# Kernel optimization log

Measured on AMD Instinct MI355X. Metric: run time of the kernel, lower is better.

Reference implementation:

```python
import jax, jax.numpy as jnp
import numpy as np

B, T, D = 16, 512, 256
HS, D_A, R = 512, 64, 8


def setup_inputs() -> dict:
    key = jax.random.key(0)
    ks = jax.random.split(key, 8)
    s = lambda *sh: 1.0 / np.sqrt(sh[0])
    x = jax.random.normal(ks[0], (B, T, D), dtype=jnp.float32)
    w_first = jax.random.normal(ks[1], (D, D_A), dtype=jnp.float32) * s(D)
    b_first = jnp.zeros((D_A,), dtype=jnp.float32)
    w_second = jax.random.normal(ks[2], (D_A, R), dtype=jnp.float32) * s(D_A)
    b_second = jnp.zeros((R,), dtype=jnp.float32)
    weight_iBarh = jax.random.normal(ks[3], (D, 4 * HS), dtype=jnp.float32) * s(D)
    weight_hh = jax.random.normal(ks[4], (HS, 4 * HS), dtype=jnp.float32) * s(HS)
    bias = jnp.zeros((4 * HS,), dtype=jnp.float32)
    return {"x": x, "w_first": w_first, "b_first": b_first,
            "w_second": w_second, "b_second": b_second,
            "weight_iBarh": weight_iBarh, "weight_hh": weight_hh, "bias": bias}


def _forward(x, w_first, b_first, w_second, b_second, weight_iBarh, weight_hh, bias):
    b, t, d = x.shape
    hs = weight_hh.shape[0]
    r = w_second.shape[1]
    # attention logits for every timestep: (B, T, r)
    s = jnp.tanh(x @ w_first + b_first) @ w_second + b_second
    # causal mask: query t attends to keys j <= t
    mask = jnp.tril(jnp.ones((t, t), dtype=bool))  # (t_query, j_key)
    # logits: (B, Tq, Tk, r); softmax over key axis per (t, r), masked to prefix
    logits = jnp.where(mask[None, :, :, None], s[:, None, :, :], -jnp.inf)
    attn = jax.nn.softmax(logits, axis=2).mean(axis=-1)  # (B, Tq, Tk) == mean over r
    # M_t = attention-weighted average of prefix inputs: (B, T, D)
    M = jnp.einsum('btj,bjd->btd', attn, x)
    gates_x = jnp.einsum('btd,dg->btg', M, weight_iBarh) + bias  # (B, T, 4H)

    def step(carry, gx):
        h, c = carry
        g = gx + h @ weight_hh  # (B, 4H)
        i = jax.nn.sigmoid(g[:, :hs])
        f = jax.nn.sigmoid(g[:, hs:2 * hs])
        gg = jnp.tanh(g[:, 2 * hs:3 * hs])
        o = jax.nn.sigmoid(g[:, 3 * hs:])
        c = f * c + i * gg
        h = o * jnp.tanh(c)
        return (h, c), h

    h0 = jnp.zeros((b, hs), dtype=x.dtype)
    c0 = jnp.zeros((b, hs), dtype=x.dtype)
    (h_t, c_t), hseq = jax.lax.scan(step, (h0, c0), jnp.swapaxes(gates_x, 0, 1))
    hidden_seq = jnp.swapaxes(hseq, 0, 1)  # (B, T, H)
    return hidden_seq, h_t, c_t


def reference(x, w_first, b_first, w_second, b_second, weight_iBarh, weight_hh, bias):
    return _forward(x, w_first, b_first, w_second, b_second, weight_iBarh, weight_hh, bias)
```

## Files before the change

### kernel.cpp

```cpp
#include <hip/hip_runtime.h>
#include <math.h>

#define BB 16
#define TT 512
#define DD 256
#define HS 512
#define DA 64
#define RR 8
#define G4H 2048


__global__ __launch_bounds__(256) void k1_score(
    const float* __restrict__ x, const float* __restrict__ w1,
    const float* __restrict__ b1, const float* __restrict__ w2,
    const float* __restrict__ b2, float* __restrict__ s_out) {
  const int wave = threadIdx.x >> 6;
  const int lane = threadIdx.x & 63;
  for (int i = 0; i < 4; ++i) {
    const int bt = blockIdx.x * 16 + wave * 4 + i;
    const float* xr = x + bt * DD;
    float acc = b1[lane];
    #pragma unroll 4
    for (int d = 0; d < DD; ++d)
      acc = fmaf(xr[d], w1[d * DA + lane], acc);
    const float a = tanhf(acc);
    #pragma unroll
    for (int r = 0; r < RR; ++r) {
      float v = a * w2[lane * RR + r];
      for (int off = 32; off > 0; off >>= 1) v += __shfl_xor(v, off);
      if (lane == 0) s_out[bt * RR + r] = v + b2[r];
    }
  }
}

__global__ __launch_bounds__(512) void k2_prefix(
    const float* __restrict__ s_in, float* __restrict__ e_out,
    float* __restrict__ inv_out) {
  const int b = blockIdx.x >> 3, r = blockIdx.x & 7;
  const int t = threadIdx.x;
  __shared__ float red[TT];
  __shared__ float buf[2][TT];
  const float v = s_in[(b * TT + t) * RR + r];
  red[t] = v;
  __syncthreads();
  for (int off = 256; off >= 1; off >>= 1) {
    if (t < off) red[t] = fmaxf(red[t], red[t + off]);
    __syncthreads();
  }
  const float m = red[0];
  const float e = expf(v - m);
  int p = 0;
  buf[0][t] = e;
  __syncthreads();
  for (int off = 1; off < TT; off <<= 1) {
    const float add = (t >= off) ? buf[p][t - off] : 0.f;
    buf[1 - p][t] = buf[p][t] + add;
    __syncthreads();
    p ^= 1;
  }
  const float den = buf[p][t];
  e_out[(b * TT + t) * RR + r] = e;
  inv_out[(b * TT + t) * RR + r] = 1.0f / den;
}

__global__ __launch_bounds__(64) void k3_mix(
    const float* __restrict__ x, const float* __restrict__ e_in,
    const float* __restrict__ inv_in, float* __restrict__ Mout) {
  const int b = blockIdx.x >> 2;
  const int d = (blockIdx.x & 3) * 64 + threadIdx.x;
  __shared__ __align__(16) float el[TT * RR];
  __shared__ __align__(16) float il[TT * RR];
  for (int i = threadIdx.x * 4; i < TT * RR; i += 64 * 4) {
    *(float4*)&el[i] = *(const float4*)&e_in[b * TT * RR + i];
    *(float4*)&il[i] = *(const float4*)&inv_in[b * TT * RR + i];
  }
  __syncthreads();
  float4 c0 = {0.f, 0.f, 0.f, 0.f}, c1 = {0.f, 0.f, 0.f, 0.f};
  for (int t = 0; t < TT; ++t) {
    const float xv = x[(b * TT + t) * DD + d];
    const float4 e0 = *(const float4*)&el[t * RR];
    const float4 e1 = *(const float4*)&el[t * RR + 4];
    const float4 i0 = *(const float4*)&il[t * RR];
    const float4 i1 = *(const float4*)&il[t * RR + 4];
    c0.x = fmaf(e0.x, xv, c0.x); c0.y = fmaf(e0.y, xv, c0.y);
    c0.z = fmaf(e0.z, xv, c0.z); c0.w = fmaf(e0.w, xv, c0.w);
    c1.x = fmaf(e1.x, xv, c1.x); c1.y = fmaf(e1.y, xv, c1.y);
    c1.z = fmaf(e1.z, xv, c1.z); c1.w = fmaf(e1.w, xv, c1.w);
    float msum = c0.x * i0.x + c0.y * i0.y + c0.z * i0.z + c0.w * i0.w;
    msum += c1.x * i1.x + c1.y * i1.y + c1.z * i1.z + c1.w * i1.w;
    Mout[(b * TT + t) * DD + d] = msum * 0.125f;
  }
}

__global__ __launch_bounds__(256) void k4_gemm(
    const float* __restrict__ A, const float* __restrict__ Bw,
    const float* __restrict__ bias, float* __restrict__ C) {
  const int bn = blockIdx.x & 15;
  const int bm = blockIdx.x >> 4;
  const int tid = threadIdx.x;
  const int tx = tid & 15, ty = tid >> 4;
  __shared__ __align__(16) float As[16][132];
  __shared__ __align__(16) float Bs[16][132];
  const int row0 = bm * 128, col0 = bn * 128;

  float acc[2][4][2][4];
  #pragma unroll
  for (int a = 0; a < 2; ++a)
    #pragma unroll
    for (int i = 0; i < 4; ++i)
      #pragma unroll
      for (int q = 0; q < 2; ++q)
        #pragma unroll
        for (int j = 0; j < 4; ++j) acc[a][i][q][j] = 0.f;

  const int arow = tid >> 1, akc = (tid & 1) * 8;
  const int bkr = tid >> 4, bcc = (tid & 15) * 8;

  for (int k0 = 0; k0 < 256; k0 += 16) {
    const float4 a0 = *(const float4*)&A[(row0 + arow) * 256 + k0 + akc];
    const float4 a1 = *(const float4*)&A[(row0 + arow) * 256 + k0 + akc + 4];
    const float4 b0 = *(const float4*)&Bw[(k0 + bkr) * 2048 + col0 + bcc];
    const float4 b1 = *(const float4*)&Bw[(k0 + bkr) * 2048 + col0 + bcc + 4];
    __syncthreads();
    As[akc + 0][arow] = a0.x; As[akc + 1][arow] = a0.y;
    As[akc + 2][arow] = a0.z; As[akc + 3][arow] = a0.w;
    As[akc + 4][arow] = a1.x; As[akc + 5][arow] = a1.y;
    As[akc + 6][arow] = a1.z; As[akc + 7][arow] = a1.w;
    *(float4*)&Bs[bkr][bcc] = b0;
    *(float4*)&Bs[bkr][bcc + 4] = b1;
    __syncthreads();
    #pragma unroll
    for (int kk = 0; kk < 16; ++kk) {
      float av[8], bv[8];
      *(float4*)&av[0] = *(const float4*)&As[kk][ty * 4];
      *(float4*)&av[4] = *(const float4*)&As[kk][64 + ty * 4];
      *(float4*)&bv[0] = *(const float4*)&Bs[kk][tx * 4];
      *(float4*)&bv[4] = *(const float4*)&Bs[kk][64 + tx * 4];
      #pragma unroll
      for (int a = 0; a < 2; ++a)
        #pragma unroll
        for (int i = 0; i < 4; ++i)
          #pragma unroll
          for (int q = 0; q < 2; ++q)
            #pragma unroll
            for (int j = 0; j < 4; ++j)
              acc[a][i][q][j] = fmaf(av[a * 4 + i], bv[q * 4 + j], acc[a][i][q][j]);
    }
  }
  const float4 bias0 = *(const float4*)&bias[col0 + tx * 4];
  const float4 bias1 = *(const float4*)&bias[col0 + 64 + tx * 4];
  #pragma unroll
  for (int a = 0; a < 2; ++a)
    #pragma unroll
    for (int i = 0; i < 4; ++i) {
      const int row = row0 + a * 64 + ty * 4 + i;
      float4 v0, v1;
      v0.x = acc[a][i][0][0] + bias0.x; v0.y = acc[a][i][0][1] + bias0.y;
      v0.z = acc[a][i][0][2] + bias0.z; v0.w = acc[a][i][0][3] + bias0.w;
      v1.x = acc[a][i][1][0] + bias1.x; v1.y = acc[a][i][1][1] + bias1.y;
      v1.z = acc[a][i][1][2] + bias1.z; v1.w = acc[a][i][1][3] + bias1.w;
      *(float4*)&C[row * 2048 + col0 + tx * 4] = v0;
      *(float4*)&C[row * 2048 + col0 + 64 + tx * 4] = v1;
    }
}

#define FMA4(ACC, W4, HSC)                         \
  ACC.x = fmaf((W4).x, (HSC), ACC.x);              \
  ACC.y = fmaf((W4).y, (HSC), ACC.y);              \
  ACC.z = fmaf((W4).z, (HSC), ACC.z);              \
  ACC.w = fmaf((W4).w, (HSC), ACC.w);

__device__ __forceinline__ float fast_sigmoid(float x) {
  return __builtin_amdgcn_rcpf(1.f + __expf(-x));
}
__device__ __forceinline__ float fast_tanh(float x) {
  const float xc = fmaxf(x, -30.f);
  const float e = __expf(-2.f * xc);
  return (1.f - e) * __builtin_amdgcn_rcpf(1.f + e);
}

__global__ __launch_bounds__(512, 1) void k5_lstm(
    const float* __restrict__ gates, const float* __restrict__ whh,
    float* __restrict__ out, unsigned long long* hbuf) {
  const int s   = blockIdx.x & 15;
  const int b   = blockIdx.x >> 4;
  const int tid = threadIdx.x;
  const int kq  = tid & 15;
  const int cq  = tid >> 4;
  const int j0  = s * 32;
  const int unit = j0 + cq;

  __shared__ __align__(16) float Wl[256 * 128];
  __shared__ __align__(16) float hl[2][576];

  float4 wr[32];
  for (int rnd = 0; rnd < 2; ++rnd) {
    for (int i = tid * 4; i < 256 * 128; i += 512 * 4) {
      const int k = i >> 7, c = i & 127;
      *(float4*)&Wl[i] =
          *(const float4*)&whh[(rnd * 256 + k) * G4H + (c >> 5) * HS + j0 + (c & 31)];
    }
    __syncthreads();
    if ((kq >> 3) == rnd) {
      const int kb = (kq & 7) * 32;
      #pragma unroll
      for (int kk = 0; kk < 32; ++kk) {
        const int base = (kb + kk) * 128 + cq;
        wr[kk].x = *(volatile const float*)&Wl[base];
        wr[kk].y = *(volatile const float*)&Wl[base + 32];
        wr[kk].z = *(volatile const float*)&Wl[base + 64];
        wr[kk].w = *(volatile const float*)&Wl[base + 96];
      }
    }
    __syncthreads();
  }

  float c_reg = 0.f;

  for (int t = 0; t < TT; ++t) {
    float gi = 0.f, gf = 0.f, gg = 0.f, go = 0.f;
    if (kq == 0) {
      const float* gt = gates + ((long)b * TT + t) * G4H + unit;
      gi = gt[0]; gf = gt[HS]; gg = gt[2 * HS]; go = gt[3 * HS];
    }
    const int par = t & 1;
    if (t > 0) {
      const unsigned long long* hsrc = hbuf + (((t - 1) & 1) * BB + b) * HS;
      unsigned long long pkt;
      do {
        pkt = __hip_atomic_load(&hsrc[tid], __ATOMIC_RELAXED,
                                __HIP_MEMORY_SCOPE_AGENT);
      } while ((unsigned)(pkt >> 32) < (unsigned)t);
      hl[par][(tid >> 5) * 36 + (tid & 31)] = __uint_as_float((unsigned)pkt);
    }
    __syncthreads();
    float4 acc = {0.f, 0.f, 0.f, 0.f};
    if (t > 0) {
      const float* hb = &hl[par][kq * 36];
      #pragma unroll
      for (int i = 0; i < 8; ++i) {
        const float4 h4 = *(const float4*)(hb + i * 4);
        FMA4(acc, wr[i * 4 + 0], h4.x);
        FMA4(acc, wr[i * 4 + 1], h4.y);
        FMA4(acc, wr[i * 4 + 2], h4.z);
        FMA4(acc, wr[i * 4 + 3], h4.w);
      }
    }
    #pragma unroll
    for (int off = 1; off <= 8; off <<= 1) {
      acc.x += __shfl_xor(acc.x, off); acc.y += __shfl_xor(acc.y, off);
      acc.z += __shfl_xor(acc.z, off); acc.w += __shfl_xor(acc.w, off);
    }
    if (kq == 0) {
      const float I = fast_sigmoid(acc.x + gi);
      const float F = fast_sigmoid(acc.y + gf);
      const float G = fast_tanh(acc.z + gg);
      const float O = fast_sigmoid(acc.w + go);
      c_reg = F * c_reg + I * G;
      const float h = O * fast_tanh(c_reg);
      const unsigned long long pkt =
          ((unsigned long long)(unsigned)(t + 1) << 32) |
          (unsigned long long)__float_as_uint(h);
      __hip_atomic_store(&hbuf[((t & 1) * BB + b) * HS + unit], pkt,
                         __ATOMIC_RELAXED, __HIP_MEMORY_SCOPE_AGENT);
      out[((long)b * TT + t) * HS + unit] = h;
      if (t == TT - 1) {
        out[(long)BB * TT * HS + b * HS + unit] = h;
        out[(long)BB * TT * HS + BB * HS + b * HS + unit] = c_reg;
      }
    }
  }
}

extern "C" void kernel_launch(void* const* d_in, const int* in_sizes, int n_in,
                              void* d_out, int out_size, void* d_ws,
                              size_t ws_size, hipStream_t stream) {
  const float* x    = (const float*)d_in[0];
  const float* w1   = (const float*)d_in[1];
  const float* b1   = (const float*)d_in[2];
  const float* w2   = (const float*)d_in[3];
  const float* b2   = (const float*)d_in[4];
  const float* wih  = (const float*)d_in[5];
  const float* whh  = (const float*)d_in[6];
  const float* bias = (const float*)d_in[7];
  float* out = (float*)d_out;

  float* ws = (float*)d_ws;
  float* s_buf  = ws;
  float* e_buf  = ws + 65536;
  float* i_buf  = ws + 131072;
  float* M_buf  = ws + 196608;
  float* g_buf  = ws + 2293760;
  unsigned long long* hbuf64 = (unsigned long long*)ws;

  k1_score<<<512, 256, 0, stream>>>(x, w1, b1, w2, b2, s_buf);
  k2_prefix<<<BB * RR, 512, 0, stream>>>(s_buf, e_buf, i_buf);
  k3_mix<<<64, 64, 0, stream>>>(x, e_buf, i_buf, M_buf);
  k4_gemm<<<64 * 16, 256, 0, stream>>>(M_buf, wih, bias, g_buf);
  hipMemsetAsync(hbuf64, 0, 2 * BB * HS * sizeof(unsigned long long), stream);
  k5_lstm<<<256, 512, 0, stream>>>(g_buf, whh, out, hbuf64);
}
```

Measured before the change: 1.143 ms.

## Pipeline LSTM gate prefetch, overlap poll loads, use packed f2 FMAs

```diff
diff --git a/kernel.cpp b/kernel.cpp
--- a/kernel.cpp
+++ b/kernel.cpp
@@ -8,6 +8,8 @@
 #define DA 64
 #define RR 8
 #define G4H 2048
+
+typedef __attribute__((ext_vector_type(2))) float f2;
 
 
 __global__ __launch_bounds__(256) void k1_score(
@@ -164,12 +166,6 @@
     }
 }
 
-#define FMA4(ACC, W4, HSC)                         \
-  ACC.x = fmaf((W4).x, (HSC), ACC.x);              \
-  ACC.y = fmaf((W4).y, (HSC), ACC.y);              \
-  ACC.z = fmaf((W4).z, (HSC), ACC.z);              \
-  ACC.w = fmaf((W4).w, (HSC), ACC.w);
-
 __device__ __forceinline__ float fast_sigmoid(float x) {
   return __builtin_amdgcn_rcpf(1.f + __expf(-x));
 }
@@ -177,6 +173,11 @@
   const float xc = fmaxf(x, -30.f);
   const float e = __expf(-2.f * xc);
   return (1.f - e) * __builtin_amdgcn_rcpf(1.f + e);
+}
+
+__device__ __forceinline__ unsigned long long poll_ld(
+    const unsigned long long* p) {
+  return __hip_atomic_load(p, __ATOMIC_RELAXED, __HIP_MEMORY_SCOPE_AGENT);
 }
 
 __global__ __launch_bounds__(512, 1) void k5_lstm(
@@ -193,7 +194,7 @@
   __shared__ __align__(16) float Wl[256 * 128];
   __shared__ __align__(16) float hl[2][576];
 
-  float4 wr[32];
+  f2 wrA[32], wrB[32];
   for (int rnd = 0; rnd < 2; ++rnd) {
     for (int i = tid * 4; i < 256 * 128; i += 512 * 4) {
       const int k = i >> 7, c = i & 127;
@@ -206,10 +207,10 @@
       #pragma unroll
       for (int kk = 0; kk < 32; ++kk) {
         const int base = (kb + kk) * 128 + cq;
-        wr[kk].x = *(volatile const float*)&Wl[base];
-        wr[kk].y = *(volatile const float*)&Wl[base + 32];
-        wr[kk].z = *(volatile const float*)&Wl[base + 64];
-        wr[kk].w = *(volatile const float*)&Wl[base + 96];
+        wrA[kk].x = *(volatile const float*)&Wl[base];
+        wrA[kk].y = *(volatile const float*)&Wl[base + 32];
+        wrB[kk].x = *(volatile const float*)&Wl[base + 64];
+        wrB[kk].y = *(volatile const float*)&Wl[base + 96];
       }
     }
     __syncthreads();
@@ -217,51 +218,69 @@
 
   float c_reg = 0.f;
 
+  float4 g_cur = {0, 0, 0, 0}, g_n1 = {0, 0, 0, 0};
+  const float* gbase = gates + (long)b * TT * G4H + unit;
+  if (kq == 0) {
+    g_cur.x = gbase[0];            g_cur.y = gbase[HS];
+    g_cur.z = gbase[2 * HS];       g_cur.w = gbase[3 * HS];
+    const float* g1 = gbase + G4H;
+    g_n1.x = g1[0];                g_n1.y = g1[HS];
+    g_n1.z = g1[2 * HS];           g_n1.w = g1[3 * HS];
+  }
+
   for (int t = 0; t < TT; ++t) {
-    float gi = 0.f, gf = 0.f, gg = 0.f, go = 0.f;
-    if (kq == 0) {
-      const float* gt = gates + ((long)b * TT + t) * G4H + unit;
-      gi = gt[0]; gf = gt[HS]; gg = gt[2 * HS]; go = gt[3 * HS];
-    }
     const int par = t & 1;
     if (t > 0) {
-      const unsigned long long* hsrc = hbuf + (((t - 1) & 1) * BB + b) * HS;
-      unsigned long long pkt;
-      do {
-        pkt = __hip_atomic_load(&hsrc[tid], __ATOMIC_RELAXED,
-                                __HIP_MEMORY_SCOPE_AGENT);
-      } while ((unsigned)(pkt >> 32) < (unsigned)t);
-      hl[par][(tid >> 5) * 36 + (tid & 31)] = __uint_as_float((unsigned)pkt);
-    }
-    __syncthreads();
-    float4 acc = {0.f, 0.f, 0.f, 0.f};
+      const unsigned long long* ha =
+          hbuf + (((t - 1) & 1) * BB + b) * HS + tid;
+      unsigned long long p0 = poll_ld(ha), p1 = poll_ld(ha);
+      unsigned long long p2 = poll_ld(ha), p3 = poll_ld(ha);
+      for (;;) {
+        if ((unsigned)(p0 >> 32) >= (unsigned)t) break;
+        p0 = p1; p1 = p2; p2 = p3; p3 = poll_ld(ha);
+      }
+      hl[par][(tid >> 5) * 36 + (tid & 31)] = __uint_as_float((unsigned)p0);
+    }
+    float4 g_n2 = {0, 0, 0, 0};
+    if (kq == 0) {
+      const int tn = (t + 2 < TT) ? t + 2 : TT - 1;
+      const float* g2 = gbase + (long)tn * G4H;
+      g_n2.x = g2[0];        g_n2.y = g2[HS];
+      g_n2.z = g2[2 * HS];   g_n2.w = g2[3 * HS];
+    }
+    __asm__ __volatile__("s_waitcnt lgkmcnt(0)\ns_barrier" ::: "memory");
+    f2 acc01 = {0.f, 0.f}, acc23 = {0.f, 0.f};
     if (t > 0) {
       const float* hb = &hl[par][kq * 36];
       #pragma unroll
       for (int i = 0; i < 8; ++i) {
         const float4 h4 = *(const float4*)(hb + i * 4);
-        FMA4(acc, wr[i * 4 + 0], h4.x);
-        FMA4(acc, wr[i * 4 + 1], h4.y);
-        FMA4(acc, wr[i * 4 + 2], h4.z);
-        FMA4(acc, wr[i * 4 + 3], h4.w);
+        const f2 hx = {h4.x, h4.x}, hy = {h4.y, h4.y};
+        const f2 hz = {h4.z, h4.z}, hw = {h4.w, h4.w};
+        acc01 += wrA[i * 4 + 0] * hx;  acc23 += wrB[i * 4 + 0] * hx;
+        acc01 += wrA[i * 4 + 1] * hy;  acc23 += wrB[i * 4 + 1] * hy;
+        acc01 += wrA[i * 4 + 2] * hz;  acc23 += wrB[i * 4 + 2] * hz;
+        acc01 += wrA[i * 4 + 3] * hw;  acc23 += wrB[i * 4 + 3] * hw;
       }
     }
     #pragma unroll
     for (int off = 1; off <= 8; off <<= 1) {
-      acc.x += __shfl_xor(acc.x, off); acc.y += __shfl_xor(acc.y, off);
-      acc.z += __shfl_xor(acc.z, off); acc.w += __shfl_xor(acc.w, off);
+      acc01.x += __shfl_xor(acc01.x, off);
+      acc01.y += __shfl_xor(acc01.y, off);
+      acc23.x += __shfl_xor(acc23.x, off);
+      acc23.y += __shfl_xor(acc23.y, off);
     }
     if (kq == 0) {
-      const float I = fast_sigmoid(acc.x + gi);
-      const float F = fast_sigmoid(acc.y + gf);
-      const float G = fast_tanh(acc.z + gg);
-      const float O = fast_sigmoid(acc.w + go);
+      const float I = fast_sigmoid(acc01.x + g_cur.x);
+      const float F = fast_sigmoid(acc01.y + g_cur.y);
+      const float G = fast_tanh(acc23.x + g_cur.z);
+      const float O = fast_sigmoid(acc23.y + g_cur.w);
       c_reg = F * c_reg + I * G;
       const float h = O * fast_tanh(c_reg);
       const unsigned long long pkt =
           ((unsigned long long)(unsigned)(t + 1) << 32) |
           (unsigned long long)__float_as_uint(h);
-      __hip_atomic_store(&hbuf[((t & 1) * BB + b) * HS + unit], pkt,
+      __hip_atomic_store(&hbuf[(par * BB + b) * HS + unit], pkt,
                          __ATOMIC_RELAXED, __HIP_MEMORY_SCOPE_AGENT);
       out[((long)b * TT + t) * HS + unit] = h;
       if (t == TT - 1) {
@@ -269,6 +288,8 @@
         out[(long)BB * TT * HS + BB * HS + b * HS + unit] = c_reg;
       }
     }
+    g_cur = g_n1;
+    g_n1 = g_n2;
   }
 }
 
```

Result: slower. 1.821 ms (+59.3%).
